# Performance work log

Hardware: AMD Instinct MI355X
Metric: run time of the kernel (lower is better)

## Reference

```python
import jax, jax.numpy as jnp
import numpy as np
import math

CS = 8       # cell_size
NBINS = 8
SIGMA = 1.0
IMG = 224
BATCH = 256
TWO_PI = 2.0 * math.pi


def setup_inputs() -> dict:
    key = jax.random.key(0)
    x = jax.random.normal(key, (BATCH, 3, IMG, IMG), dtype=jnp.float32)
    coords = jnp.arange(CS, dtype=jnp.float32) - (CS - 1) / 2.0
    xx, yy = jnp.meshgrid(coords, coords, indexing='ij')
    gauss = jnp.exp(-(xx ** 2 + yy ** 2) / (2.0 * SIGMA ** 2)).reshape(1, CS * CS)
    kx = jnp.array([[-1., 0., 1.], [-2., 0., 2.], [-1., 0., 1.]], dtype=jnp.float32).reshape(1, 1, 3, 3)
    ky = jnp.array([[-1., -2., -1.], [0., 0., 0.], [1., 2., 1.]], dtype=jnp.float32).reshape(1, 1, 3, 3)
    return {"x": x, "gauss": gauss, "kx": kx, "ky": ky}


def _conv(im, k):
    # NCHW conv, padding=1, stride=1 (matches F.conv2d(..., padding=1))
    return jax.lax.conv_general_dilated(
        im, k, window_strides=(1, 1), padding=[(1, 1), (1, 1)],
        dimension_numbers=('NCHW', 'OIHW', 'NCHW'))


def reference(x, gauss, kx, ky):
    bs, _, H, W = x.shape
    gray = 0.2989 * x[:, 0:1] + 0.587 * x[:, 1:2] + 0.114 * x[:, 2:3]  # [bs,1,H,W]
    gx = _conv(gray, kx)
    gy = _conv(gray, ky)
    mag = jnp.sqrt(gx ** 2 + gy ** 2 + 1e-6)
    ang = jnp.mod(jnp.arctan2(gy, gx), TWO_PI)
    Hc, Wc = H // CS, W // CS
    n_cells = Hc * Wc

    def to_cells(a):
        # [bs,1,H,W] -> [bs*n_cells, CS*CS], within-cell order (kh,kw) row-major
        # matching F.unfold's kernel-position ordering.
        return a.reshape(bs, Hc, CS, Wc, CS).transpose(0, 1, 3, 2, 4).reshape(bs * n_cells, CS * CS)

    mags = to_cells(mag) * gauss  # gauss broadcasts over kernel positions
    angs = to_cells(ang)

    bin_w = TWO_PI / NBINS
    idx = (angs / bin_w).astype(jnp.int32) % NBINS  # [bs*n_cells, CS*CS]

    N = bs * n_cells
    hist = jnp.zeros((N, NBINS), dtype=mags.dtype)
    hist = hist.at[jnp.arange(N)[:, None], idx].add(mags)  # scatter_add per cell
    hist = hist.reshape(bs, n_cells * NBINS)
    hist = hist / (jnp.linalg.norm(hist, axis=1, keepdims=True) + 1e-6)
    return hist
```

## Files before the change

kernel.cpp:

```cpp
#include <hip/hip_runtime.h>
#include <math.h>

#define NBINS 8
#define IMG 224
#define HC 28
#define OUTPER (HC*HC*NBINS)
#define BATCH 256
#define PL (IMG*IMG)

typedef float v4f __attribute__((ext_vector_type(4)));

__device__ __forceinline__ float dpp_swap1(float x) {
    return __int_as_float(__builtin_amdgcn_update_dpp(
        0, __float_as_int(x), 0xB1, 0xF, 0xF, false));
}

template<bool EDGE>
__device__ __forceinline__ void load_gray(const float* __restrict__ xb,
                                          int r0, int col4, int lane,
                                          float4 v[10])
{
    #pragma unroll
    for (int j = 0; j < 10; ++j) {
        int gr  = r0 - 1 + j;
        int grc = EDGE ? (gr < 0 ? 0 : (gr > IMG - 1 ? IMG - 1 : gr)) : gr;
        const v4f* p = (const v4f*)(xb + grc * IMG + col4);
        v4f R = __builtin_nontemporal_load(p);
        v4f G = __builtin_nontemporal_load(p + PL / 4);
        v4f B = __builtin_nontemporal_load(p + 2 * (PL / 4));
        float4 g;
        g.x = 0.2989f * R.x + 0.587f * G.x + 0.114f * B.x;
        g.y = 0.2989f * R.y + 0.587f * G.y + 0.114f * B.y;
        g.z = 0.2989f * R.z + 0.587f * G.z + 0.114f * B.z;
        g.w = 0.2989f * R.w + 0.587f * G.w + 0.114f * B.w;
        bool z = (lane >= 56) || (EDGE && (gr < 0 || gr > IMG - 1));
        if (z) { g.x = 0.f; g.y = 0.f; g.z = 0.f; g.w = 0.f; }
        v[j] = g;
    }
}

__global__ __launch_bounds__(256) void hog_main_kernel(
    const float* __restrict__ x, float* __restrict__ out,
    float* __restrict__ partial)
{
    const int tid  = threadIdx.x;
    const int wv   = tid >> 6;
    const int lane = tid & 63;
    const int b    = blockIdx.y;
    const int cr   = blockIdx.x * 4 + wv;
    const int r0   = cr * 8;
    const int li   = lane < 55 ? lane : 55;
    const int col4 = li * 4;

    const float* xb = x + (size_t)b * 3 * PL;

    float4 v[10];
    if (cr == 0 || cr == HC - 1) load_gray<true >(xb, r0, col4, lane, v);
    else                         load_gray<false>(xb, r0, col4, lane, v);

    const float E0 = 0.0021874911f, E1 = 0.043936934f,
                E2 = 0.32465247f,   E3 = 0.88249690f;
    const bool odd = (lane & 1);
    const float ew0 = odd ? E3 : E0, ew1 = odd ? E2 : E1,
                ew2 = odd ? E1 : E2, ew3 = odd ? E0 : E3;
    const float EROW[8] = { E0, E1, E2, E3, E3, E2, E1, E0 };

    float h[8];
    #pragma unroll
    for (int k = 0; k < 8; ++k) h[k] = 0.f;

    auto pix = [&](float gx, float gy, float w) {
        float mag = __builtin_amdgcn_sqrtf(gx * gx + gy * gy + 1e-6f);
        float ax = fabsf(gx), ay = fabsf(gy);
        int bin;
        if (gy > 0.f)       bin = (gx > 0.f)  ? ((gy < gx) ? 0 : 1)
                                : (gx == 0.f) ? 2 : ((ay > ax) ? 2 : 3);
        else if (gy == 0.f) bin = (gx < 0.f) ? 4 : 0;
        else                bin = (gx < 0.f)  ? ((ay < ax) ? 4 : 5)
                                : (gx == 0.f) ? 6 : ((ay > ax) ? 6 : 7);
        float wm = w * mag;
        #pragma unroll
        for (int k = 0; k < 8; ++k) h[k] += (bin == k) ? wm : 0.f;
    };

    #pragma unroll
    for (int sr = 0; sr < 8; ++sr) {
        float4 t = v[sr], m = v[sr + 1], bt = v[sr + 2];
        float4 s, d;
        s.x = t.x + 2.f * m.x + bt.x;  s.y = t.y + 2.f * m.y + bt.y;
        s.z = t.z + 2.f * m.z + bt.z;  s.w = t.w + 2.f * m.w + bt.w;
        d.x = bt.x - t.x;  d.y = bt.y - t.y;
        d.z = bt.z - t.z;  d.w = bt.w - t.w;

        float sL = __shfl_up(s.w, 1, 64);   sL = (lane == 0) ? 0.f : sL;
        float dL = __shfl_up(d.w, 1, 64);   dL = (lane == 0) ? 0.f : dL;
        float sR = __shfl_down(s.x, 1, 64);
        float dR = __shfl_down(d.x, 1, 64);

        float gx0 = s.y - sL,  gx1 = s.z - s.x,
              gx2 = s.w - s.y, gx3 = sR  - s.z;
        float gy0 = dL  + 2.f * d.x + d.y, gy1 = d.x + 2.f * d.y + d.z,
              gy2 = d.y + 2.f * d.z + d.w, gy3 = d.z + 2.f * d.w + dR;

        float er = EROW[sr];
        pix(gx0, gy0, er * ew0);
        pix(gx1, gy1, er * ew1);
        pix(gx2, gy2, er * ew2);
        pix(gx3, gy3, er * ew3);
    }

    #pragma unroll
    for (int k = 0; k < 8; ++k) h[k] += dpp_swap1(h[k]);

    float ssq = 0.f;
    if (lane < 56) {
        float4 st = odd ? make_float4(h[4], h[5], h[6], h[7])
                        : make_float4(h[0], h[1], h[2], h[3]);
        *(float4*)(out + (size_t)b * OUTPER + (size_t)cr * IMG + 4 * lane) = st;
        ssq = st.x * st.x + st.y * st.y + st.z * st.z + st.w * st.w;
    }

    #pragma unroll
    for (int o = 32; o > 0; o >>= 1) ssq += __shfl_down(ssq, o, 64);
    if (lane == 0) partial[b * HC + cr] = ssq;
}

__global__ __launch_bounds__(256) void hog_norm_kernel(
    float* __restrict__ out, const float* __restrict__ partial)
{
    const int bq = blockIdx.x, tid = threadIdx.x;
    const int b = bq >> 2, q = bq & 3;
    __shared__ float wsum[4];
    __shared__ float s_inv;
    float s = (tid < HC) ? partial[b * HC + tid] : 0.f;
    #pragma unroll
    for (int o = 32; o > 0; o >>= 1) s += __shfl_down(s, o, 64);
    if ((tid & 63) == 0) wsum[tid >> 6] = s;
    __syncthreads();
    if (tid == 0) {
        float t = wsum[0] + wsum[1] + wsum[2] + wsum[3];
        s_inv = 1.0f / (sqrtf(t) + 1e-6f);
    }
    __syncthreads();
    float inv = s_inv;
    float4* o4 = (float4*)(out + (size_t)b * OUTPER + (size_t)q * (OUTPER / 4));
    for (int i = tid; i < OUTPER / 16; i += 256) {
        float4 w = o4[i];
        w.x *= inv; w.y *= inv; w.z *= inv; w.w *= inv;
        o4[i] = w;
    }
}

extern "C" void kernel_launch(void* const* d_in, const int* in_sizes, int n_in,
                              void* d_out, int out_size, void* d_ws, size_t ws_size,
                              hipStream_t stream) {
    const float* x = (const float*)d_in[0];
    float* out     = (float*)d_out;
    float* partial = (float*)d_ws;

    hog_main_kernel<<<dim3(7, BATCH), 256, 0, stream>>>(x, out, partial);
    hog_norm_kernel<<<BATCH * 4, 256, 0, stream>>>(out, partial);
}
```

Baseline: 225.9 us.

## Process two cell rows per wave to share halo rows and stage loads

Each wave now handles a pair of adjacent cell rows, loading 18 input rows instead of 2×10, so the halo rows between the two cells are read once instead of twice. The loads are split into two batches separated by sched_barriers, so part of the gray conversion runs while the second batch is in flight. Blocks shrink to 128 threads and the partial-sum array drops to 14 entries per image. The cost is more live registers per thread (up to 18 float4 plus staged RGB arrays), which may lower occupancy.

After: 238.4 us. +5.5%, slower.

```diff
diff --git a/kernel.cpp b/kernel.cpp
--- a/kernel.cpp
+++ b/kernel.cpp
@@ -7,6 +7,7 @@
 #define OUTPER (HC*HC*NBINS)
 #define BATCH 256
 #define PL (IMG*IMG)
+#define NPAIR 14
 
 typedef float v4f __attribute__((ext_vector_type(4)));
 
@@ -15,54 +16,14 @@
         0, __float_as_int(x), 0xB1, 0xF, 0xF, false));
 }
 
-template<bool EDGE>
-__device__ __forceinline__ void load_gray(const float* __restrict__ xb,
-                                          int r0, int col4, int lane,
-                                          float4 v[10])
+template<int BASE>
+__device__ __forceinline__ float cell_row(
+    const float4 (&v)[18], int lane, bool live,
+    float ew0, float ew1, float ew2, float ew3,
+    float* __restrict__ outp)
 {
-    #pragma unroll
-    for (int j = 0; j < 10; ++j) {
-        int gr  = r0 - 1 + j;
-        int grc = EDGE ? (gr < 0 ? 0 : (gr > IMG - 1 ? IMG - 1 : gr)) : gr;
-        const v4f* p = (const v4f*)(xb + grc * IMG + col4);
-        v4f R = __builtin_nontemporal_load(p);
-        v4f G = __builtin_nontemporal_load(p + PL / 4);
-        v4f B = __builtin_nontemporal_load(p + 2 * (PL / 4));
-        float4 g;
-        g.x = 0.2989f * R.x + 0.587f * G.x + 0.114f * B.x;
-        g.y = 0.2989f * R.y + 0.587f * G.y + 0.114f * B.y;
-        g.z = 0.2989f * R.z + 0.587f * G.z + 0.114f * B.z;
-        g.w = 0.2989f * R.w + 0.587f * G.w + 0.114f * B.w;
-        bool z = (lane >= 56) || (EDGE && (gr < 0 || gr > IMG - 1));
-        if (z) { g.x = 0.f; g.y = 0.f; g.z = 0.f; g.w = 0.f; }
-        v[j] = g;
-    }
-}
-
-__global__ __launch_bounds__(256) void hog_main_kernel(
-    const float* __restrict__ x, float* __restrict__ out,
-    float* __restrict__ partial)
-{
-    const int tid  = threadIdx.x;
-    const int wv   = tid >> 6;
-    const int lane = tid & 63;
-    const int b    = blockIdx.y;
-    const int cr   = blockIdx.x * 4 + wv;
-    const int r0   = cr * 8;
-    const int li   = lane < 55 ? lane : 55;
-    const int col4 = li * 4;
-
-    const float* xb = x + (size_t)b * 3 * PL;
-
-    float4 v[10];
-    if (cr == 0 || cr == HC - 1) load_gray<true >(xb, r0, col4, lane, v);
-    else                         load_gray<false>(xb, r0, col4, lane, v);
-
     const float E0 = 0.0021874911f, E1 = 0.043936934f,
                 E2 = 0.32465247f,   E3 = 0.88249690f;
-    const bool odd = (lane & 1);
-    const float ew0 = odd ? E3 : E0, ew1 = odd ? E2 : E1,
-                ew2 = odd ? E1 : E2, ew3 = odd ? E0 : E3;
     const float EROW[8] = { E0, E1, E2, E3, E3, E2, E1, E0 };
 
     float h[8];
@@ -85,7 +46,7 @@
 
     #pragma unroll
     for (int sr = 0; sr < 8; ++sr) {
-        float4 t = v[sr], m = v[sr + 1], bt = v[sr + 2];
+        float4 t = v[BASE + sr], m = v[BASE + sr + 1], bt = v[BASE + sr + 2];
         float4 s, d;
         s.x = t.x + 2.f * m.x + bt.x;  s.y = t.y + 2.f * m.y + bt.y;
         s.z = t.z + 2.f * m.z + bt.z;  s.w = t.w + 2.f * m.w + bt.w;
@@ -113,16 +74,99 @@
     for (int k = 0; k < 8; ++k) h[k] += dpp_swap1(h[k]);
 
     float ssq = 0.f;
-    if (lane < 56) {
+    if (live) {
+        bool odd = (lane & 1);
         float4 st = odd ? make_float4(h[4], h[5], h[6], h[7])
                         : make_float4(h[0], h[1], h[2], h[3]);
-        *(float4*)(out + (size_t)b * OUTPER + (size_t)cr * IMG + 4 * lane) = st;
+        *(float4*)outp = st;
         ssq = st.x * st.x + st.y * st.y + st.z * st.z + st.w * st.w;
     }
+    return ssq;
+}
+
+__global__ __launch_bounds__(128) void hog_main_kernel(
+    const float* __restrict__ x, float* __restrict__ out,
+    float* __restrict__ partial)
+{
+    const int tid  = threadIdx.x;
+    const int wv   = tid >> 6;
+    const int lane = tid & 63;
+    const int b    = blockIdx.y;
+    const int crp  = blockIdx.x * 2 + wv;
+    const int cr0  = crp * 2;
+    const int r0   = cr0 * 8;
+    const int li   = lane < 55 ? lane : 55;
+    const int col4 = li * 4;
+
+    const float* base = x + (size_t)b * 3 * PL + col4;
+    const bool edge = (crp == 0) || (crp == NPAIR - 1);
+
+    float4 v[18];
+
+    auto run = [&](auto EDGEC) {
+        constexpr bool EDGE = decltype(EDGEC)::value;
+        int off[18];
+        #pragma unroll
+        for (int j = 0; j < 18; ++j) {
+            int gr  = r0 - 1 + j;
+            int grc = EDGE ? (gr < 0 ? 0 : (gr > IMG - 1 ? IMG - 1 : gr)) : gr;
+            off[j] = grc * IMG;
+        }
+        auto cvt = [&](int j, v4f R, v4f G, v4f B) {
+            float4 g;
+            g.x = 0.2989f * R.x + 0.587f * G.x + 0.114f * B.x;
+            g.y = 0.2989f * R.y + 0.587f * G.y + 0.114f * B.y;
+            g.z = 0.2989f * R.z + 0.587f * G.z + 0.114f * B.z;
+            g.w = 0.2989f * R.w + 0.587f * G.w + 0.114f * B.w;
+            int gr = r0 - 1 + j;
+            bool z = (lane >= 56) || (EDGE && (gr < 0 || gr > IMG - 1));
+            if (z) { g.x = 0.f; g.y = 0.f; g.z = 0.f; g.w = 0.f; }
+            v[j] = g;
+        };
+
+        v4f RA[10], GA[10], BA[10];
+        #pragma unroll
+        for (int j = 0; j < 10; ++j) {
+            const v4f* p = (const v4f*)(base + off[j]);
+            RA[j] = __builtin_nontemporal_load(p);
+            GA[j] = __builtin_nontemporal_load(p + PL / 4);
+            BA[j] = __builtin_nontemporal_load(p + 2 * (PL / 4));
+        }
+        __builtin_amdgcn_sched_barrier(0);
+        #pragma unroll
+        for (int j = 0; j < 6; ++j) cvt(j, RA[j], GA[j], BA[j]);
+        __builtin_amdgcn_sched_barrier(0);
+        v4f RB[8], GB[8], BB[8];
+        #pragma unroll
+        for (int j = 0; j < 8; ++j) {
+            const v4f* p = (const v4f*)(base + off[10 + j]);
+            RB[j] = __builtin_nontemporal_load(p);
+            GB[j] = __builtin_nontemporal_load(p + PL / 4);
+            BB[j] = __builtin_nontemporal_load(p + 2 * (PL / 4));
+        }
+        __builtin_amdgcn_sched_barrier(0);
+        #pragma unroll
+        for (int j = 6; j < 10; ++j) cvt(j, RA[j], GA[j], BA[j]);
+        #pragma unroll
+        for (int j = 0; j < 8; ++j) cvt(10 + j, RB[j], GB[j], BB[j]);
+    };
+    if (edge) run(std::integral_constant<bool, true>{});
+    else      run(std::integral_constant<bool, false>{});
+
+    const float E0 = 0.0021874911f, E1 = 0.043936934f,
+                E2 = 0.32465247f,   E3 = 0.88249690f;
+    const bool odd = (lane & 1);
+    const float ew0 = odd ? E3 : E0, ew1 = odd ? E2 : E1,
+                ew2 = odd ? E1 : E2, ew3 = odd ? E0 : E3;
+
+    const bool live = (lane < 56);
+    float* outA = out + (size_t)b * OUTPER + (size_t)cr0 * IMG + 4 * li;
+    float ssq  = cell_row<0>(v, lane, live, ew0, ew1, ew2, ew3, outA);
+    ssq       += cell_row<8>(v, lane, live, ew0, ew1, ew2, ew3, outA + IMG);
 
     #pragma unroll
     for (int o = 32; o > 0; o >>= 1) ssq += __shfl_down(ssq, o, 64);
-    if (lane == 0) partial[b * HC + cr] = ssq;
+    if (lane == 0) partial[b * NPAIR + crp] = ssq;
 }
 
 __global__ __launch_bounds__(256) void hog_norm_kernel(
@@ -132,7 +176,7 @@
     const int b = bq >> 2, q = bq & 3;
     __shared__ float wsum[4];
     __shared__ float s_inv;
-    float s = (tid < HC) ? partial[b * HC + tid] : 0.f;
+    float s = (tid < NPAIR) ? partial[b * NPAIR + tid] : 0.f;
     #pragma unroll
     for (int o = 32; o > 0; o >>= 1) s += __shfl_down(s, o, 64);
     if ((tid & 63) == 0) wsum[tid >> 6] = s;
@@ -158,6 +202,6 @@
     float* out     = (float*)d_out;
     float* partial = (float*)d_ws;
 
-    hog_main_kernel<<<dim3(7, BATCH), 256, 0, stream>>>(x, out, partial);
+    hog_main_kernel<<<dim3(7, BATCH), 128, 0, stream>>>(x, out, partial);
     hog_norm_kernel<<<BATCH * 4, 256, 0, stream>>>(out, partial);
 }
```
